# Kernel tuning notes

Measured on AMD Instinct MI355X. Metric: run time of the kernel, lower is better.

Reference implementation:

```python
import jax, jax.numpy as jnp
import numpy as np

B, S, D, H, DFF = 2, 2048, 768, 12, 3072
DK = D // H
EPS = 1e-6
NEG = -1e9


def setup_inputs() -> dict:
    key = jax.random.key(0)
    ks = jax.random.split(key, 16)
    s = 1.0 / np.sqrt(D)
    inp = {
        'x': jax.random.normal(ks[0], (B, S, D), jnp.float32),
        'wq': jax.random.normal(ks[1], (D, D), jnp.float32) * s,
        'bq': jnp.zeros((D,), jnp.float32),
        'wk': jax.random.normal(ks[2], (D, D), jnp.float32) * s,
        'bk': jnp.zeros((D,), jnp.float32),
        'wv': jax.random.normal(ks[3], (D, D), jnp.float32) * s,
        'bv': jnp.zeros((D,), jnp.float32),
        'wo': jax.random.normal(ks[4], (D, D), jnp.float32) * s,
        'bo': jnp.zeros((D,), jnp.float32),
        'w1': jax.random.normal(ks[5], (D, DFF), jnp.float32) * s,
        'b1': jnp.zeros((DFF,), jnp.float32),
        'w2': jax.random.normal(ks[6], (DFF, D), jnp.float32) * (1.0 / np.sqrt(DFF)),
        'b2': jnp.zeros((D,), jnp.float32),
        'alpha1': jnp.ones((1,), jnp.float32),
        'beta1': jnp.zeros((1,), jnp.float32),
        'alpha2': jnp.ones((1,), jnp.float32),
        'beta2': jnp.zeros((1,), jnp.float32),
        'mask': jax.random.randint(ks[7], (1, 1, S, S), 0, 2, jnp.int32),
    }
    return inp


def layernorm(x, alpha, beta):
    # torch: mean and UNBIASED std (ddof=1), eps added to std (not variance)
    mean = jnp.mean(x, axis=-1, keepdims=True)
    std = jnp.std(x, axis=-1, keepdims=True, ddof=1)
    return alpha * (x - mean) / (std + EPS) + beta


def encoder_layer(x, wq, bq, wk, bk, wv, bv, wo, bo, w1, b1, w2, b2,
                  alpha1, beta1, alpha2, beta2, mask):
    # projections -> [B, H, S, DK]
    def split_heads(t):
        return t.reshape(B, S, H, DK).transpose(0, 2, 1, 3)
    q = split_heads(x @ wq + bq)
    k = split_heads(x @ wk + bk)
    v = split_heads(x @ wv + bv)
    scores = jnp.einsum('bhqd,bhkd->bhqk', q, k) / np.sqrt(DK)  # [B,H,S,S]
    scores = jnp.where(mask == 0, NEG, scores)
    attn = jax.nn.softmax(scores, axis=-1)
    ctx = jnp.einsum('bhqk,bhkd->bhqd', attn, v)
    ctx = ctx.transpose(0, 2, 1, 3).reshape(B, S, D)
    attn_out = ctx @ wo + bo
    x = layernorm(x + attn_out, alpha1, beta1)
    ff = jax.nn.relu(x @ w1 + b1) @ w2 + b2
    x = layernorm(x + ff, alpha2, beta2)
    return x


def reference(x, wq, bq, wk, bk, wv, bv, wo, bo, w1, b1, w2, b2,
              alpha1, beta1, alpha2, beta2, mask):
    return encoder_layer(x, wq, bq, wk, bk, wv, bv, wo, bo, w1, b1, w2, b2,
                         alpha1, beta1, alpha2, beta2, mask)
```

## Files before the change

### kernel.cpp

```cpp
#include <hip/hip_runtime.h>
#include <hip/hip_bf16.h>


typedef short short8 __attribute__((ext_vector_type(8)));
typedef float floatx4 __attribute__((ext_vector_type(4)));
typedef unsigned short ushort_t;
typedef ushort_t ushort4_t __attribute__((ext_vector_type(4)));

#define B_ 2
#define S_ 2048
#define D_ 768
#define H_ 12
#define DK_ 64
#define DFF_ 3072
#define M_ (B_ * S_)
#define RS_ (3 * D_)

#define LOG2E 1.44269504f
#define FMAX_SHIFT 16.0f

__device__ __forceinline__ float bf2f(ushort_t h) {
  union { unsigned int u; float f; } v; v.u = ((unsigned int)h) << 16; return v.f;
}
__device__ __forceinline__ ushort_t f2bf(float f) {
  union { float f; unsigned int u; } v; v.f = f;
  unsigned int u = v.u;
  unsigned int r = (u + 0x7fffu + ((u >> 16) & 1u)) >> 16;
  return (ushort_t)r;
}

__global__ __launch_bounds__(256) void transpose_all_f2b(
    const float* __restrict__ wq, const float* __restrict__ wk,
    const float* __restrict__ wv, const float* __restrict__ wo,
    const float* __restrict__ w1, const float* __restrict__ w2,
    ushort_t* __restrict__ wTqkv, ushort_t* __restrict__ woT,
    ushort_t* __restrict__ w1T, ushort_t* __restrict__ w2T) {
  __shared__ ushort_t t[32][33];
  const int blk = blockIdx.x;
  const float* in; ushort_t* out; int K, N, bx, by;
  if (blk < 2304) {
    const int z = blk / 576, rr = blk % 576;
    in = (z == 0) ? wq : (z == 1) ? wk : (z == 2) ? wv : wo;
    out = (z < 3) ? (wTqkv + (size_t)z * D_ * D_) : woT;
    K = D_; N = D_; bx = rr % 24; by = rr / 24;
  } else if (blk < 4608) {
    const int rr = blk - 2304;
    in = w1; out = w1T; K = D_; N = DFF_; bx = rr % 96; by = rr / 96;
  } else {
    const int rr = blk - 4608;
    in = w2; out = w2T; K = DFF_; N = D_; bx = rr % 24; by = rr / 24;
  }
  const int nt = bx * 32, kt = by * 32;
  const int tx = threadIdx.x & 31, ty = threadIdx.x >> 5;
#pragma unroll
  for (int i = 0; i < 4; i++)
    t[ty + i * 8][tx] = f2bf(in[(size_t)(kt + ty + i * 8) * N + nt + tx]);
  __syncthreads();
#pragma unroll
  for (int i = 0; i < 4; i++)
    out[(size_t)(nt + ty + i * 8) * K + kt + tx] = t[tx][ty + i * 8];
}

__global__ __launch_bounds__(256) void prep_misc(
    const int* __restrict__ mask, ushort_t* __restrict__ maskp,
    const float* __restrict__ x, ushort_t* __restrict__ xb,
    const float* __restrict__ bq, const float* __restrict__ bk,
    const float* __restrict__ bv, float* __restrict__ bqkv) {
  const int blk = blockIdx.x, tid = threadIdx.x;
  if (blk < 2048) {
    const int t = blk * 256 + tid;
    const int q = t >> 8;
    const int cc = t & 255;
    const int k0 = (cc >> 3) * 64;
    const int g = cc & 7, f = g >> 2, lq = g & 3;
    const int* mrow = mask + (size_t)q * S_ + k0;
    const ushort_t cm = f2bf(-1.4427e9f);
    const ushort_t cu = f2bf(-FMAX_SHIFT * LOG2E);
    short8 o;
#pragma unroll
    for (int n2 = 0; n2 < 2; n2++)
#pragma unroll
      for (int r = 0; r < 4; r++) {
        const int kpl = 32 * f + 16 * n2 + 4 * lq + r;
        o[n2 * 4 + r] = (short)((mrow[kpl] == 0) ? cm : cu);
      }
    *(short8*)(maskp + (size_t)q * S_ + k0 + g * 8) = o;
  } else if (blk < 5120) {
    const int i = ((blk - 2048) * 256 + tid) * 4;
#pragma unroll
    for (int j = 0; j < 4; j++) xb[i + j] = f2bf(x[i + j]);
  } else {
    const int i = (blk - 5120) * 256 + tid;
    if (i < 3 * D_)
      bqkv[i] = (i < D_) ? bq[i] : (i < 2 * D_ ? bk[i - D_] : bv[i - 2 * D_]);
  }
}

template <int BN, bool SPLIT, bool VOUT>
__global__ __launch_bounds__(256) void gemm_bt_t(
    const ushort_t* __restrict__ A, const ushort_t* __restrict__ Bt,
    const float* __restrict__ bias, void* __restrict__ Cv,
    ushort_t* __restrict__ vtout,
    int M, int N, int K, int relu, int qcols, float qscale) {
  constexpr int WN = (BN == 128) ? 2 : 1;
  constexpr int WM = 4 / WN;
  constexpr int FI = 128 / WM / 16;
  constexpr int FJ = BN / WN / 16;
  constexpr int Z = SPLIT ? 2 : 1;
  __shared__ __align__(16) ushort_t Al[2][128 * 32];
  __shared__ __align__(16) ushort_t Bl[2][BN * 32];
  const int tid = threadIdx.x;
  const int w = tid >> 6, lane = tid & 63;
  const int wm = (WN == 2) ? (w >> 1) : w;
  const int wn = (WN == 2) ? (w & 1) : 0;
  const int lq = lane >> 4, lr = lane & 15;

  const int NT_n = N / BN;
  const int mg = M >> 10;
  const int lin = blockIdx.x;
  const int xcd = lin & 7, idx = lin >> 3;
  const int m_t = xcd * mg + idx / (NT_n * Z);
  const int rem = idx % (NT_n * Z);
  const int n_t = rem % NT_n;
  const int z   = rem / NT_n;
  const int m0 = m_t * 128, n0 = n_t * BN;

  int kBeg = 0, kEnd = K;
  if (SPLIT) { const int half = K >> 1; kBeg = z * half; kEnd = kBeg + half; }
  const int NT = (kEnd - kBeg) / 32;

  auto stage = [&](int kt, int s) {
    const int k0 = kBeg + kt * 32;
#pragma unroll
    for (int i = 0; i < 2; i++) {
      const int base = (w * 2 + i) * 512;
      const int e = base + lane * 8;
      const int row = e >> 5, col = e & 31;
      __builtin_amdgcn_global_load_lds(
          (const __attribute__((address_space(1))) void*)(A + (size_t)(m0 + row) * K + k0 + col),
          (__attribute__((address_space(3))) void*)(&Al[s][base]), 16, 0, 0);
    }
#pragma unroll
    for (int i = 0; i < BN / 64; i++) {
      const int base = (w * (BN / 64) + i) * 512;
      const int e = base + lane * 8;
      const int row = e >> 5, col = e & 31;
      __builtin_amdgcn_global_load_lds(
          (const __attribute__((address_space(1))) void*)(Bt + (size_t)(n0 + row) * K + k0 + col),
          (__attribute__((address_space(3))) void*)(&Bl[s][base]), 16, 0, 0);
    }
  };

  floatx4 acc[FI][FJ];
#pragma unroll
  for (int i = 0; i < FI; i++)
#pragma unroll
    for (int j = 0; j < FJ; j++) acc[i][j] = (floatx4){0.f, 0.f, 0.f, 0.f};

  stage(0, 0);
  for (int kt = 0; kt < NT; kt++) {
    const int s = kt & 1;
    __syncthreads();
    if (kt + 1 < NT) stage(kt + 1, s ^ 1);

    short8 af[FI], bf[FJ];
#pragma unroll
    for (int i = 0; i < FI; i++)
      af[i] = *(const short8*)&Al[s][(wm * (FI * 16) + i * 16 + lr) * 32 + lq * 8];
#pragma unroll
    for (int j = 0; j < FJ; j++)
      bf[j] = *(const short8*)&Bl[s][(wn * (FJ * 16) + j * 16 + lr) * 32 + lq * 8];
#pragma unroll
    for (int i = 0; i < FI; i++)
#pragma unroll
      for (int j = 0; j < FJ; j++)
        acc[i][j] = __builtin_amdgcn_mfma_f32_16x16x32_bf16(af[i], bf[j], acc[i][j], 0, 0, 0);
  }

#pragma unroll
  for (int i = 0; i < FI; i++) {
    const int m = m0 + wm * (FI * 16) + i * 16 + lq * 4;
#pragma unroll
    for (int j = 0; j < FJ; j++) {
      const int n = n0 + wn * (FJ * 16) + j * 16 + lr;
      if (SPLIT) {
        ushort_t* P = (ushort_t*)Cv + (size_t)z * M * N;
#pragma unroll
        for (int r = 0; r < 4; r++)
          P[(size_t)(m + r) * N + n] = f2bf(acc[i][j][r]);
      } else if (VOUT && n >= 2 * D_) {
        const int h = (n - 2 * D_) >> 6, d = (n - 2 * D_) & 63;
        const int bh = (m >> 11) * H_ + h;
        const int kp = m & (S_ - 1);
        const int kw = kp & 63;
        const int pos = (kp & ~63) + ((kw >> 5) << 5) + (((kw >> 2) & 3) << 3)
                      + (((kw >> 4) & 1) << 2);
        const float bv = bias[n];
        ushort4_t o;
#pragma unroll
        for (int r = 0; r < 4; r++) o[r] = f2bf(acc[i][j][r] + bv);
        *(ushort4_t*)(vtout + ((size_t)bh * DK_ + d) * S_ + pos) = o;
      } else {
        const float bv = bias[n];
#pragma unroll
        for (int r = 0; r < 4; r++) {
          float v = acc[i][j][r] + bv;
          if (n < qcols) v *= qscale;
          if (relu) v = v > 0.f ? v : 0.f;
          ((ushort_t*)Cv)[(size_t)(m + r) * N + n] = f2bf(v);
        }
      }
    }
  }
}

__global__ __launch_bounds__(256, 3) void flash_attn(
    const ushort_t* __restrict__ qkv, const ushort_t* __restrict__ vt,
    const ushort_t* __restrict__ maskp, ushort_t* __restrict__ ctx) {
  __shared__ __align__(16) ushort_t lds[2][3][64 * 64];
  const int tid = threadIdx.x;
  const int w = tid >> 6, lane = tid & 63;
  const int wq = w >> 1, wk = w & 1;
  const int lq = lane >> 4, lr = lane & 15;
  const int blk = blockIdx.x;
  const int bh = blk % (B_ * H_), qb = blk / (B_ * H_);
  const int b = bh / H_, h = bh % H_;
  const int q0 = qb * 64;
  const ushort_t* qbase = qkv + (size_t)(b * S_) * RS_ + h * DK_;
  const ushort_t* kbase = qbase + D_;
  const ushort_t* vtb   = vt + (size_t)bh * DK_ * S_;
  const ushort_t* mb    = maskp + (size_t)q0 * S_;

  short8 qfr[2][2];
#pragma unroll
  for (int qf = 0; qf < 2; qf++)
#pragma unroll
    for (int f = 0; f < 2; f++)
      qfr[qf][f] = *(const short8*)(
          qbase + (size_t)(q0 + wq * 32 + qf * 16 + lr) * RS_ + f * 32 + lq * 8);

  auto stage = [&](int k0, int s) {
#pragma unroll
    for (int i = 0; i < 2; i++) {
      const int id = i * 256 + tid;
      const int row = id >> 3;
      const int cc = ((id & 7) ^ (row & 7)) * 8;
      const int dbase = (i * 256 + w * 64) * 8;
      __builtin_amdgcn_global_load_lds(
          (const __attribute__((address_space(1))) void*)(kbase + (size_t)(k0 + row) * RS_ + cc),
          (__attribute__((address_space(3))) void*)(&lds[s][0][dbase]), 16, 0, 0);
      __builtin_amdgcn_global_load_lds(
          (const __attribute__((address_space(1))) void*)(vtb + (size_t)row * S_ + k0 + cc),
          (__attribute__((address_space(3))) void*)(&lds[s][1][dbase]), 16, 0, 0);
      __builtin_amdgcn_global_load_lds(
          (const __attribute__((address_space(1))) void*)(mb + (size_t)row * S_ + k0 + cc),
          (__attribute__((address_space(3))) void*)(&lds[s][2][dbase]), 16, 0, 0);
    }
  };

  floatx4 oacc[2][4], oli[2];
#pragma unroll
  for (int qf = 0; qf < 2; qf++) {
    oli[qf] = (floatx4){0.f, 0.f, 0.f, 0.f};
#pragma unroll
    for (int dt = 0; dt < 4; dt++) oacc[qf][dt] = (floatx4){0.f, 0.f, 0.f, 0.f};
  }
  short8 ones;
#pragma unroll
  for (int j = 0; j < 8; j++) ones[j] = (short)0x3F80;

  stage(0, 0);
  __syncthreads();

  const int sw8 = lr & 7;
  const int c0 = (lq ^ sw8) * 8;
  const int c1 = ((4 + lq) ^ sw8) * 8;
  const int cW = ((4 * wk + lq) ^ sw8) * 8;

  constexpr int NT = S_ / 64;
  for (int t = 0; t < NT; t++) {
    const int s = t & 1;
    if (t + 1 < NT) stage((t + 1) * 64, s ^ 1);

    const ushort_t* kl = &lds[s][0][0];
    const ushort_t* vl = &lds[s][1][0];
    const ushort_t* ml = &lds[s][2][0];

    floatx4 sacc[2][2];
#pragma unroll
    for (int qf = 0; qf < 2; qf++) {
      const short8 bb = *(const short8*)(ml + (wq * 32 + qf * 16 + lr) * 64 + cW);
#pragma unroll
      for (int n2 = 0; n2 < 2; n2++)
#pragma unroll
        for (int r = 0; r < 4; r++)
          sacc[qf][n2][r] = bf2f((ushort_t)bb[n2 * 4 + r]);
    }

#pragma unroll
    for (int n2 = 0; n2 < 2; n2++) {
      const int krow = ((2 * wk + n2) * 16 + lr) * 64;
      short8 a0 = *(const short8*)(kl + krow + c0);
      short8 a1 = *(const short8*)(kl + krow + c1);
#pragma unroll
      for (int qf = 0; qf < 2; qf++) {
        sacc[qf][n2] = __builtin_amdgcn_mfma_f32_16x16x32_bf16(a0, qfr[qf][0], sacc[qf][n2], 0, 0, 0);
        sacc[qf][n2] = __builtin_amdgcn_mfma_f32_16x16x32_bf16(a1, qfr[qf][1], sacc[qf][n2], 0, 0, 0);
      }
    }

    short8 pf[2];
#pragma unroll
    for (int qf = 0; qf < 2; qf++) {
      union { __hip_bfloat162 h2[4]; short8 v; } u;
#pragma unroll
      for (int jj = 0; jj < 4; jj++) {
        const int e0 = jj * 2, e1 = jj * 2 + 1;
        float2 p2;
        p2.x = __builtin_amdgcn_exp2f(sacc[qf][e0 >> 2][e0 & 3]);
        p2.y = __builtin_amdgcn_exp2f(sacc[qf][e1 >> 2][e1 & 3]);
        u.h2[jj] = __float22bfloat162_rn(p2);
      }
      pf[qf] = u.v;
    }

#pragma unroll
    for (int dt = 0; dt < 4; dt++) {
      const short8 vfr = *(const short8*)(vl + (dt * 16 + lr) * 64 + cW);
#pragma unroll
      for (int qf = 0; qf < 2; qf++)
        oacc[qf][dt] = __builtin_amdgcn_mfma_f32_16x16x32_bf16(vfr, pf[qf], oacc[qf][dt], 0, 0, 0);
    }
#pragma unroll
    for (int qf = 0; qf < 2; qf++)
      oli[qf] = __builtin_amdgcn_mfma_f32_16x16x32_bf16(ones, pf[qf], oli[qf], 0, 0, 0);

    __syncthreads();
  }

  float* ex = (float*)&lds[0][0][0];
  if (wk == 1) {
    float* dst = ex + (size_t)(wq * 64 + lane) * 37;
#pragma unroll
    for (int qf = 0; qf < 2; qf++)
#pragma unroll
      for (int dt = 0; dt < 4; dt++)
#pragma unroll
        for (int r = 0; r < 4; r++)
          dst[qf * 16 + dt * 4 + r] = oacc[qf][dt][r];
    dst[32] = oli[0][0];
    dst[33] = oli[1][0];
  }
  __syncthreads();
  if (wk == 0) {
    const float* src = ex + (size_t)(wq * 64 + lane) * 37;
#pragma unroll
    for (int qf = 0; qf < 2; qf++)
#pragma unroll
      for (int dt = 0; dt < 4; dt++)
#pragma unroll
        for (int r = 0; r < 4; r++)
          oacc[qf][dt][r] += src[qf * 16 + dt * 4 + r];
    const float inv0 = 1.f / (oli[0][0] + src[32] + 1e-30f);
    const float inv1 = 1.f / (oli[1][0] + src[33] + 1e-30f);
#pragma unroll
    for (int qf = 0; qf < 2; qf++) {
      const float inv = qf ? inv1 : inv0;
      const size_t row = (size_t)(b * S_ + q0 + wq * 32 + qf * 16 + lr) * D_ + h * DK_;
#pragma unroll
      for (int dt = 0; dt < 4; dt++) {
        ushort4_t o;
#pragma unroll
        for (int r = 0; r < 4; r++) o[r] = f2bf(oacc[qf][dt][r] * inv);
        *(ushort4_t*)(ctx + row + dt * 16 + lq * 4) = o;
      }
    }
  }
}

template <bool XF, bool OF>
__global__ __launch_bounds__(256) void add_ln_comb(
    const void* __restrict__ xv, const ushort_t* __restrict__ P0,
    const ushort_t* __restrict__ P1, const float* __restrict__ cb,
    const float* __restrict__ alpha, const float* __restrict__ beta,
    void* __restrict__ outv) {
  const int row = blockIdx.x, tid = threadIdx.x;
  const int w = tid >> 6, lane = tid & 63;
  __shared__ float red[8];
  float v[3];
#pragma unroll
  for (int i = 0; i < 3; i++) {
    const int c = tid + i * 256;
    const size_t idx = (size_t)row * D_ + c;
    float xv_;
    if (XF) xv_ = ((const float*)xv)[idx];
    else    xv_ = bf2f(((const ushort_t*)xv)[idx]);
    v[i] = xv_ + (bf2f(P0[idx]) + bf2f(P1[idx]) + cb[c]);
  }
  float s = v[0] + v[1] + v[2];
#pragma unroll
  for (int off = 1; off < 64; off <<= 1) s += __shfl_xor(s, off);
  if (lane == 0) red[w] = s;
  __syncthreads();
  const float mean = (red[0] + red[1] + red[2] + red[3]) / (float)D_;
  float d = 0.f;
#pragma unroll
  for (int i = 0; i < 3; i++) { const float t = v[i] - mean; d += t * t; }
#pragma unroll
  for (int off = 1; off < 64; off <<= 1) d += __shfl_xor(d, off);
  if (lane == 0) red[4 + w] = d;
  __syncthreads();
  const float var = (red[4] + red[5] + red[6] + red[7]) / (float)(D_ - 1);
  const float inv = 1.f / (sqrtf(var) + 1e-6f);
  const float a = alpha[0] * inv, bt = beta[0];
#pragma unroll
  for (int i = 0; i < 3; i++) {
    const int c = tid + i * 256;
    const float o = a * (v[i] - mean) + bt;
    if (OF) ((float*)outv)[(size_t)row * D_ + c] = o;
    else    ((ushort_t*)outv)[(size_t)row * D_ + c] = f2bf(o);
  }
}

extern "C" void kernel_launch(void* const* d_in, const int* in_sizes, int n_in,
                              void* d_out, int out_size, void* d_ws, size_t ws_size,
                              hipStream_t stream) {
  const float* x   = (const float*)d_in[0];
  const float* wq  = (const float*)d_in[1];
  const float* bq  = (const float*)d_in[2];
  const float* wk  = (const float*)d_in[3];
  const float* bk  = (const float*)d_in[4];
  const float* wv  = (const float*)d_in[5];
  const float* bv  = (const float*)d_in[6];
  const float* wo  = (const float*)d_in[7];
  const float* bo  = (const float*)d_in[8];
  const float* w1  = (const float*)d_in[9];
  const float* b1  = (const float*)d_in[10];
  const float* w2  = (const float*)d_in[11];
  const float* b2  = (const float*)d_in[12];
  const float* a1  = (const float*)d_in[13];
  const float* be1 = (const float*)d_in[14];
  const float* a2  = (const float*)d_in[15];
  const float* be2 = (const float*)d_in[16];
  const int*   msk = (const int*)d_in[17];

  const size_t E_xb    = 0;
  const size_t E_wTqkv = E_xb    + (size_t)M_ * D_;
  const size_t E_woT   = E_wTqkv + (size_t)3 * D_ * D_;
  const size_t E_w1T   = E_woT   + (size_t)D_ * D_;
  const size_t E_w2T   = E_w1T   + (size_t)DFF_ * D_;
  const size_t E_bqkv  = E_w2T   + (size_t)D_ * DFF_;
  const size_t E_qkv   = E_bqkv  + (size_t)2 * 3 * D_;
  const size_t E_ctx   = E_qkv   + (size_t)M_ * 3 * D_;
  const size_t E_attn  = E_ctx   + (size_t)M_ * D_;
  const size_t E_x1    = E_attn  + (size_t)M_ * D_;
  const size_t E_h1    = E_x1    + (size_t)M_ * D_;
  const size_t E_ff    = E_h1    + (size_t)M_ * DFF_;
  const size_t E_total = E_ff    + (size_t)M_ * D_;
  if (ws_size < E_total * sizeof(ushort_t)) return;

  ushort_t* ws    = (ushort_t*)d_ws;
  ushort_t* xb    = ws + E_xb;
  ushort_t* wTqkv = ws + E_wTqkv;
  ushort_t* woT   = ws + E_woT;
  ushort_t* w1T   = ws + E_w1T;
  ushort_t* w2T   = ws + E_w2T;
  float*    bqkv  = (float*)(ws + E_bqkv);
  ushort_t* qkv   = ws + E_qkv;
  ushort_t* ctx   = ws + E_ctx;
  ushort_t* x1    = ws + E_x1;
  ushort_t* h1    = ws + E_h1;
  ushort_t* maskp = ws + E_h1;
  ushort_t* vt    = ws + E_h1 + (size_t)S_ * S_;
  ushort_t* Pattn = ws + E_h1;
  ushort_t* Pff2  = ws + E_qkv;

  const float SCALE_Q = 0.125f * LOG2E;

  transpose_all_f2b<<<6912, 256, 0, stream>>>(wq, wk, wv, wo, w1, w2,
                                              wTqkv, woT, w1T, w2T);
  prep_misc<<<5129, 256, 0, stream>>>(msk, maskp, x, xb, bq, bk, bv, bqkv);

  gemm_bt_t<64, false, true><<<1152, 256, 0, stream>>>(
      xb, wTqkv, bqkv, qkv, vt, M_, 3 * D_, D_, 0, D_, SCALE_Q);
  flash_attn<<<(B_ * H_) * (S_ / 64), 256, 0, stream>>>(qkv, vt, maskp, ctx);
  gemm_bt_t<64, true, false><<<768, 256, 0, stream>>>(
      ctx, woT, nullptr, Pattn, nullptr, M_, D_, D_, 0, 0, 1.f);
  add_ln_comb<false, false><<<M_, 256, 0, stream>>>(
      xb, Pattn, Pattn + (size_t)M_ * D_, bo, a1, be1, x1);
  gemm_bt_t<128, false, false><<<768, 256, 0, stream>>>(
      x1, w1T, b1, h1, nullptr, M_, DFF_, D_, 1, 0, 1.f);
  gemm_bt_t<64, true, false><<<768, 256, 0, stream>>>(
      h1, w2T, nullptr, Pff2, nullptr, M_, D_, DFF_, 0, 0, 1.f);
  add_ln_comb<false, true><<<M_, 256, 0, stream>>>(
      x1, Pff2, Pff2 + (size_t)M_ * D_, b2, a2, be2, d_out);
}
```

Before: 293.2 us.

## Merge prep kernels, split-K by four, and load attention mask directly into registers

Fuses the weight-transpose and misc-prep kernels into one launch. Raises split-K for the output projection and FFN2 GEMMs from 2 to 4 partitions, doubling the grid and generalising the layernorm combine to sum four partials. Flash attention stops staging the mask tile through LDS and instead prefetches each lane's mask fragment straight from global into registers one tile ahead, cutting LDS use. More partials add memory traffic, and the workspace must hold four partial buffers, which aliasing over h1 and qkv may not fit.

```diff
diff --git a/kernel.cpp b/kernel.cpp
--- a/kernel.cpp
+++ b/kernel.cpp
@@ -29,48 +29,45 @@
   return (ushort_t)r;
 }
 
-__global__ __launch_bounds__(256) void transpose_all_f2b(
+__global__ __launch_bounds__(256) void prep_all(
     const float* __restrict__ wq, const float* __restrict__ wk,
     const float* __restrict__ wv, const float* __restrict__ wo,
     const float* __restrict__ w1, const float* __restrict__ w2,
     ushort_t* __restrict__ wTqkv, ushort_t* __restrict__ woT,
-    ushort_t* __restrict__ w1T, ushort_t* __restrict__ w2T) {
-  __shared__ ushort_t t[32][33];
-  const int blk = blockIdx.x;
-  const float* in; ushort_t* out; int K, N, bx, by;
-  if (blk < 2304) {
-    const int z = blk / 576, rr = blk % 576;
-    in = (z == 0) ? wq : (z == 1) ? wk : (z == 2) ? wv : wo;
-    out = (z < 3) ? (wTqkv + (size_t)z * D_ * D_) : woT;
-    K = D_; N = D_; bx = rr % 24; by = rr / 24;
-  } else if (blk < 4608) {
-    const int rr = blk - 2304;
-    in = w1; out = w1T; K = D_; N = DFF_; bx = rr % 96; by = rr / 96;
-  } else {
-    const int rr = blk - 4608;
-    in = w2; out = w2T; K = DFF_; N = D_; bx = rr % 24; by = rr / 24;
-  }
-  const int nt = bx * 32, kt = by * 32;
-  const int tx = threadIdx.x & 31, ty = threadIdx.x >> 5;
-#pragma unroll
-  for (int i = 0; i < 4; i++)
-    t[ty + i * 8][tx] = f2bf(in[(size_t)(kt + ty + i * 8) * N + nt + tx]);
-  __syncthreads();
-#pragma unroll
-  for (int i = 0; i < 4; i++)
-    out[(size_t)(nt + ty + i * 8) * K + kt + tx] = t[tx][ty + i * 8];
-}
-
-__global__ __launch_bounds__(256) void prep_misc(
+    ushort_t* __restrict__ w1T, ushort_t* __restrict__ w2T,
     const int* __restrict__ mask, ushort_t* __restrict__ maskp,
     const float* __restrict__ x, ushort_t* __restrict__ xb,
     const float* __restrict__ bq, const float* __restrict__ bk,
     const float* __restrict__ bv, float* __restrict__ bqkv) {
+  __shared__ ushort_t t[32][33];
   const int blk = blockIdx.x, tid = threadIdx.x;
-  if (blk < 2048) {
-    const int t = blk * 256 + tid;
-    const int q = t >> 8;
-    const int cc = t & 255;
+  if (blk < 6912) {
+    const float* in; ushort_t* out; int K, N, bx, by;
+    if (blk < 2304) {
+      const int z = blk / 576, rr = blk % 576;
+      in = (z == 0) ? wq : (z == 1) ? wk : (z == 2) ? wv : wo;
+      out = (z < 3) ? (wTqkv + (size_t)z * D_ * D_) : woT;
+      K = D_; N = D_; bx = rr % 24; by = rr / 24;
+    } else if (blk < 4608) {
+      const int rr = blk - 2304;
+      in = w1; out = w1T; K = D_; N = DFF_; bx = rr % 96; by = rr / 96;
+    } else {
+      const int rr = blk - 4608;
+      in = w2; out = w2T; K = DFF_; N = D_; bx = rr % 24; by = rr / 24;
+    }
+    const int nt = bx * 32, kt = by * 32;
+    const int tx = tid & 31, ty = tid >> 5;
+#pragma unroll
+    for (int i = 0; i < 4; i++)
+      t[ty + i * 8][tx] = f2bf(in[(size_t)(kt + ty + i * 8) * N + nt + tx]);
+    __syncthreads();
+#pragma unroll
+    for (int i = 0; i < 4; i++)
+      out[(size_t)(nt + ty + i * 8) * K + kt + tx] = t[tx][ty + i * 8];
+  } else if (blk < 8960) {
+    const int tt = (blk - 6912) * 256 + tid;
+    const int q = tt >> 8;
+    const int cc = tt & 255;
     const int k0 = (cc >> 3) * 64;
     const int g = cc & 7, f = g >> 2, lq = g & 3;
     const int* mrow = mask + (size_t)q * S_ + k0;
@@ -85,18 +82,18 @@
         o[n2 * 4 + r] = (short)((mrow[kpl] == 0) ? cm : cu);
       }
     *(short8*)(maskp + (size_t)q * S_ + k0 + g * 8) = o;
-  } else if (blk < 5120) {
-    const int i = ((blk - 2048) * 256 + tid) * 4;
+  } else if (blk < 12032) {
+    const int i = ((blk - 8960) * 256 + tid) * 4;
 #pragma unroll
     for (int j = 0; j < 4; j++) xb[i + j] = f2bf(x[i + j]);
   } else {
-    const int i = (blk - 5120) * 256 + tid;
+    const int i = (blk - 12032) * 256 + tid;
     if (i < 3 * D_)
       bqkv[i] = (i < D_) ? bq[i] : (i < 2 * D_ ? bk[i - D_] : bv[i - 2 * D_]);
   }
 }
 
-template <int BN, bool SPLIT, bool VOUT>
+template <int BN, int Z, bool VOUT>
 __global__ __launch_bounds__(256) void gemm_bt_t(
     const ushort_t* __restrict__ A, const ushort_t* __restrict__ Bt,
     const float* __restrict__ bias, void* __restrict__ Cv,
@@ -106,7 +103,7 @@
   constexpr int WM = 4 / WN;
   constexpr int FI = 128 / WM / 16;
   constexpr int FJ = BN / WN / 16;
-  constexpr int Z = SPLIT ? 2 : 1;
+  constexpr bool SPLIT = (Z > 1);
   __shared__ __align__(16) ushort_t Al[2][128 * 32];
   __shared__ __align__(16) ushort_t Bl[2][BN * 32];
   const int tid = threadIdx.x;
@@ -126,7 +123,7 @@
   const int m0 = m_t * 128, n0 = n_t * BN;
 
   int kBeg = 0, kEnd = K;
-  if (SPLIT) { const int half = K >> 1; kBeg = z * half; kEnd = kBeg + half; }
+  if (SPLIT) { const int part = K / Z; kBeg = z * part; kEnd = kBeg + part; }
   const int NT = (kEnd - kBeg) / 32;
 
   auto stage = [&](int kt, int s) {
@@ -217,7 +214,7 @@
 __global__ __launch_bounds__(256, 3) void flash_attn(
     const ushort_t* __restrict__ qkv, const ushort_t* __restrict__ vt,
     const ushort_t* __restrict__ maskp, ushort_t* __restrict__ ctx) {
-  __shared__ __align__(16) ushort_t lds[2][3][64 * 64];
+  __shared__ __align__(16) ushort_t lds[2][2][64 * 64];
   const int tid = threadIdx.x;
   const int w = tid >> 6, lane = tid & 63;
   const int wq = w >> 1, wk = w & 1;
@@ -229,7 +226,7 @@
   const ushort_t* qbase = qkv + (size_t)(b * S_) * RS_ + h * DK_;
   const ushort_t* kbase = qbase + D_;
   const ushort_t* vtb   = vt + (size_t)bh * DK_ * S_;
-  const ushort_t* mb    = maskp + (size_t)q0 * S_;
+  const ushort_t* mrow = maskp + (size_t)(q0 + wq * 32 + lr) * S_ + (4 * wk + lq) * 8;
 
   short8 qfr[2][2];
 #pragma unroll
@@ -252,9 +249,6 @@
       __builtin_amdgcn_global_load_lds(
           (const __attribute__((address_space(1))) void*)(vtb + (size_t)row * S_ + k0 + cc),
           (__attribute__((address_space(3))) void*)(&lds[s][1][dbase]), 16, 0, 0);
-      __builtin_amdgcn_global_load_lds(
-          (const __attribute__((address_space(1))) void*)(mb + (size_t)row * S_ + k0 + cc),
-          (__attribute__((address_space(3))) void*)(&lds[s][2][dbase]), 16, 0, 0);
     }
   };
 
@@ -268,6 +262,11 @@
   short8 ones;
 #pragma unroll
   for (int j = 0; j < 8; j++) ones[j] = (short)0x3F80;
+
+  short8 bb[2], bbn[2];
+#pragma unroll
+  for (int qf = 0; qf < 2; qf++)
+    bb[qf] = *(const short8*)(mrow + (size_t)qf * 16 * S_);
 
   stage(0, 0);
   __syncthreads();
@@ -280,22 +279,24 @@
   constexpr int NT = S_ / 64;
   for (int t = 0; t < NT; t++) {
     const int s = t & 1;
-    if (t + 1 < NT) stage((t + 1) * 64, s ^ 1);
+    if (t + 1 < NT) {
+      stage((t + 1) * 64, s ^ 1);
+#pragma unroll
+      for (int qf = 0; qf < 2; qf++)
+        bbn[qf] = *(const short8*)(mrow + (size_t)qf * 16 * S_ + (t + 1) * 64);
+    }
 
     const ushort_t* kl = &lds[s][0][0];
     const ushort_t* vl = &lds[s][1][0];
-    const ushort_t* ml = &lds[s][2][0];
 
     floatx4 sacc[2][2];
 #pragma unroll
-    for (int qf = 0; qf < 2; qf++) {
-      const short8 bb = *(const short8*)(ml + (wq * 32 + qf * 16 + lr) * 64 + cW);
+    for (int qf = 0; qf < 2; qf++)
 #pragma unroll
       for (int n2 = 0; n2 < 2; n2++)
 #pragma unroll
         for (int r = 0; r < 4; r++)
-          sacc[qf][n2][r] = bf2f((ushort_t)bb[n2 * 4 + r]);
-    }
+          sacc[qf][n2][r] = bf2f((ushort_t)bb[qf][n2 * 4 + r]);
 
 #pragma unroll
     for (int n2 = 0; n2 < 2; n2++) {
@@ -335,6 +336,10 @@
     for (int qf = 0; qf < 2; qf++)
       oli[qf] = __builtin_amdgcn_mfma_f32_16x16x32_bf16(ones, pf[qf], oli[qf], 0, 0, 0);
 
+    if (t + 1 < NT) {
+      bb[0] = bbn[0];
+      bb[1] = bbn[1];
+    }
     __syncthreads();
   }
 
@@ -378,10 +383,10 @@
   }
 }
 
-template <bool XF, bool OF>
+template <int NP, bool XF, bool OF>
 __global__ __launch_bounds__(256) void add_ln_comb(
-    const void* __restrict__ xv, const ushort_t* __restrict__ P0,
-    const ushort_t* __restrict__ P1, const float* __restrict__ cb,
+    const void* __restrict__ xv, const ushort_t* __restrict__ P,
+    const float* __restrict__ cb,
     const float* __restrict__ alpha, const float* __restrict__ beta,
     void* __restrict__ outv) {
   const int row = blockIdx.x, tid = threadIdx.x;
@@ -395,7 +400,10 @@
     float xv_;
     if (XF) xv_ = ((const float*)xv)[idx];
     else    xv_ = bf2f(((const ushort_t*)xv)[idx]);
-    v[i] = xv_ + (bf2f(P0[idx]) + bf2f(P1[idx]) + cb[c]);
+    float ps = cb[c];
+#pragma unroll
+    for (int p = 0; p < NP; p++) ps += bf2f(P[idx + (size_t)p * M_ * D_]);
+    v[i] = xv_ + ps;
   }
   float s = v[0] + v[1] + v[2];
 #pragma unroll
@@ -477,21 +485,21 @@
 
   const float SCALE_Q = 0.125f * LOG2E;
 
-  transpose_all_f2b<<<6912, 256, 0, stream>>>(wq, wk, wv, wo, w1, w2,
-                                              wTqkv, woT, w1T, w2T);
-  prep_misc<<<5129, 256, 0, stream>>>(msk, maskp, x, xb, bq, bk, bv, bqkv);
-
-  gemm_bt_t<64, false, true><<<1152, 256, 0, stream>>>(
+  prep_all<<<12041, 256, 0, stream>>>(wq, wk, wv, wo, w1, w2,
+                                      wTqkv, woT, w1T, w2T,
+                                      msk, maskp, x, xb, bq, bk, bv, bqkv);
+
+  gemm_bt_t<64, 1, true><<<1152, 256, 0, stream>>>(
       xb, wTqkv, bqkv, qkv, vt, M_, 3 * D_, D_, 0, D_, SCALE_Q);
   flash_attn<<<(B_ * H_) * (S_ / 64), 256, 0, stream>>>(qkv, vt, maskp, ctx);
-  gemm_bt_t<64, true, false><<<768, 256, 0, stream>>>(
+  gemm_bt_t<64, 4, false><<<1536, 256, 0, stream>>>(
       ctx, woT, nullptr, Pattn, nullptr, M_, D_, D_, 0, 0, 1.f);
-  add_ln_comb<false, false><<<M_, 256, 0, stream>>>(
-      xb, Pattn, Pattn + (size_t)M_ * D_, bo, a1, be1, x1);
-  gemm_bt_t<128, false, false><<<768, 256, 0, stream>>>(
+  add_ln_comb<4, false, false><<<M_, 256, 0, stream>>>(
+      xb, Pattn, bo, a1, be1, x1);
+  gemm_bt_t<128, 1, false><<<768, 256, 0, stream>>>(
       x1, w1T, b1, h1, nullptr, M_, DFF_, D_, 1, 0, 1.f);
-  gemm_bt_t<64, true, false><<<768, 256, 0, stream>>>(
+  gemm_bt_t<64, 4, false><<<1536, 256, 0, stream>>>(
       h1, w2T, nullptr, Pff2, nullptr, M_, D_, DFF_, 0, 0, 1.f);
-  add_ln_comb<false, true><<<M_, 256, 0, stream>>>(
-      x1, Pff2, Pff2 + (size_t)M_ * D_, b2, a2, be2, d_out);
-}
+  add_ln_comb<4, false, true><<<M_, 256, 0, stream>>>(
+      x1, Pff2, b2, a2, be2, d_out);
+}
```

Result: slower. 303.9 us (+3.6%).
